# Kernel tuning notes

Hardware: AMD Instinct MI355X
Metric: run time of the kernel (lower is better)

The kernel has to match this reference:

```python
import jax, jax.numpy as jnp
import numpy as np
from jax import lax

SIGMA = 4.0
KS = 2 * int(4.0 * SIGMA + 0.5) + 1  # 33
PAD = KS // 2  # 16


def _gaussian_kernel2d():
    half = (KS - 1) * 0.5
    x = jnp.linspace(-half, half, KS)
    pdf = jnp.exp(-0.5 * (x / SIGMA) ** 2)
    k1 = pdf / pdf.sum()
    # outer product -> dense 2D kernel, shape [O=1, I=1, KS, KS]
    return (k1[:, None] * k1[None, :])[None, None].astype(jnp.float32)


def setup_inputs() -> dict:
    key = jax.random.key(0)
    patch_scores = jax.random.normal(key, (32, 1, 28, 28), dtype=jnp.float32)
    return {
        "patch_scores": patch_scores,
        "blur_w": _gaussian_kernel2d(),
        "img_h": 512,
        "img_w": 512,
    }


def reference(patch_scores, blur_w, img_h, img_w):
    B, C, h, w = patch_scores.shape
    # F.interpolate default mode='nearest': src = floor(dst * in / out)
    ih = (jnp.arange(img_h) * h) // img_h
    iw = (jnp.arange(img_w) * w) // img_w
    x = patch_scores[:, :, ih][:, :, :, iw]  # [B, 1, img_h, img_w]
    # dense 33x33 Gaussian blur conv, padding 16 (same as nn.Conv2d)
    anomaly_map = lax.conv_general_dilated(
        x, blur_w,
        window_strides=(1, 1),
        padding=[(PAD, PAD), (PAD, PAD)],
        dimension_numbers=("NCHW", "OIHW", "NCHW"),
    )
    # mean over channel dim (dim is removed, matching torch.mean(axis=1))
    return anomaly_map.mean(axis=1)  # [B, img_h, img_w]
```

## Files before the change

### kernel.cpp

```cpp
#include <hip/hip_runtime.h>

#define IMG 512
#define PS  28
#define KS  33
#define PAD 16
#define RT  16
#define TILES (IMG / RT)

__device__ __forceinline__ int base_of(int y) {
    int p0 = y - PAD; if (p0 < 0) p0 = 0;
    int b = (p0 * PS) >> 9;
    return b > PS - 3 ? PS - 3 : b;
}

__device__ __forceinline__ float3 collapse(int y, int base, const float* S) {
    float w[3];
#pragma unroll
    for (int d = 0; d < 3; ++d) {
        int s  = base + d;
        int lo = (512 * s + 27) / 28 - y + PAD;
        int hi = (512 * (s + 1) + 27) / 28 - y + PAD;
        lo = min(max(lo, 0), KS);
        hi = min(max(hi, 0), KS);
        w[d] = S[hi] - S[lo];
    }
    return make_float3(w[0], w[1], w[2]);
}

__global__ __launch_bounds__(256) void anomaly_fused(
        const float* __restrict__ p_in,
        const float* __restrict__ blur_w,
        float* __restrict__ out) {
    __shared__ float  S[KS + 1];
    __shared__ __align__(16) float P[PS * PS];
    __shared__ float4 WY[RT];
    __shared__ __align__(16) float N[4][IMG];

    int t    = threadIdx.x;
    int b    = blockIdx.x >> 5;
    int tile = blockIdx.x & (TILES - 1);
    int y0   = tile * RT;
    int smin = base_of(y0);

    if (t < 64) {
        float v = (t < KS) ? blur_w[t * KS + 16] : 0.f;
        float c = __shfl(v, 16);
        float k = v / sqrtf(c);
        float s = k;
#pragma unroll
        for (int d = 1; d <= 32; d <<= 1) {
            float o = __shfl_up(s, (unsigned)d);
            if (t >= d) s += o;
        }
        if (t < KS)  S[t + 1] = s;
        if (t == 33) S[0] = 0.f;
    }
    if (t < (PS * PS) / 4)
        ((float4*)P)[t] = ((const float4*)(p_in + (size_t)b * PS * PS))[t];
    __syncthreads();

    if (t < RT) {
        int by = base_of(y0 + t);
        float3 w = collapse(y0 + t, by, S);
        int  dy = by - smin;
        float u0 = dy ? 0.f : w.x;
        float u1 = dy ? w.x : w.y;
        float u2 = dy ? w.y : w.z;
        float u3 = dy ? w.z : 0.f;
        WY[t] = make_float4(u0, u1, u2, u3);
    }
#pragma unroll
    for (int xi = 0; xi < 2; ++xi) {
        int x = t + xi * 256;
        int bx = base_of(x);
        float3 w = collapse(x, bx, S);
#pragma unroll
        for (int i = 0; i < 4; ++i) {
            int sr = smin + i; if (sr > PS - 1) sr = PS - 1;
            const float* pr = P + sr * PS + bx;
            N[i][x] = w.x * pr[0] + w.y * pr[1] + w.z * pr[2];
        }
    }
    __syncthreads();

    int q    = t & 127;
    int half = t >> 7;
    int x0   = q * 4;

    float4 a0 = *(const float4*)&N[0][x0];
    float4 a1 = *(const float4*)&N[1][x0];
    float4 a2 = *(const float4*)&N[2][x0];
    float4 a3 = *(const float4*)&N[3][x0];

    float* obase = out + ((size_t)b * IMG + y0 + half * 8) * IMG + x0;
#pragma unroll
    for (int r = 0; r < 8; ++r) {
        float4 u = WY[half * 8 + r];
        float4 acc;
        acc.x = u.x * a0.x + u.y * a1.x + u.z * a2.x + u.w * a3.x;
        acc.y = u.x * a0.y + u.y * a1.y + u.z * a2.y + u.w * a3.y;
        acc.z = u.x * a0.z + u.y * a1.z + u.z * a2.z + u.w * a3.z;
        acc.w = u.x * a0.w + u.y * a1.w + u.z * a2.w + u.w * a3.w;
        *(float4*)(obase + (size_t)r * IMG) = acc;
    }
}

extern "C" void kernel_launch(void* const* d_in, const int* in_sizes, int n_in,
                              void* d_out, int out_size, void* d_ws, size_t ws_size,
                              hipStream_t stream) {
    const float* patch = (const float*)d_in[0];
    const float* blur  = (const float*)d_in[1];
    float*       out   = (float*)d_out;

    int B = in_sizes[0] / (PS * PS);
    anomaly_fused<<<B * TILES, 256, 0, stream>>>(patch, blur, out);
}
```

Before: 13.64 us.

## Drop intermediate shared buffer and a barrier; compute row weights via shuffles

Removes the N[4][512] shared-memory intermediate and one __syncthreads. Row weights are now built with wave shuffles straight from the prefix-sum registers, and each thread computes its own four horizontal-collapsed values directly from the patch tile. The output stores become nontemporal. Each thread does somewhat more redundant weight and index arithmetic, with both block halves recomputing the same columns, in exchange for fewer barriers and less LDS traffic.

```diff
diff --git a/kernel.cpp b/kernel.cpp
--- a/kernel.cpp
+++ b/kernel.cpp
@@ -7,24 +7,18 @@
 #define RT  16
 #define TILES (IMG / RT)
 
+typedef float vf4 __attribute__((ext_vector_type(4)));
+
 __device__ __forceinline__ int base_of(int y) {
     int p0 = y - PAD; if (p0 < 0) p0 = 0;
     int b = (p0 * PS) >> 9;
     return b > PS - 3 ? PS - 3 : b;
 }
-
-__device__ __forceinline__ float3 collapse(int y, int base, const float* S) {
-    float w[3];
-#pragma unroll
-    for (int d = 0; d < 3; ++d) {
-        int s  = base + d;
-        int lo = (512 * s + 27) / 28 - y + PAD;
-        int hi = (512 * (s + 1) + 27) / 28 - y + PAD;
-        lo = min(max(lo, 0), KS);
-        hi = min(max(hi, 0), KS);
-        w[d] = S[hi] - S[lo];
-    }
-    return make_float3(w[0], w[1], w[2]);
+__device__ __forceinline__ int C_of(int s) {
+    return (512 * s + 27) / 28;
+}
+__device__ __forceinline__ int clamp33(int i) {
+    return min(max(i, 0), KS);
 }
 
 __global__ __launch_bounds__(256) void anomaly_fused(
@@ -34,7 +28,6 @@
     __shared__ float  S[KS + 1];
     __shared__ __align__(16) float P[PS * PS];
     __shared__ float4 WY[RT];
-    __shared__ __align__(16) float N[4][IMG];
 
     int t    = threadIdx.x;
     int b    = blockIdx.x >> 5;
@@ -42,43 +35,38 @@
     int y0   = tile * RT;
     int smin = base_of(y0);
 
+    if (t < (PS * PS) / 4)
+        ((float4*)P)[t] = ((const float4*)(p_in + (size_t)b * PS * PS))[t];
+
     if (t < 64) {
         float v = (t < KS) ? blur_w[t * KS + 16] : 0.f;
         float c = __shfl(v, 16);
-        float k = v / sqrtf(c);
-        float s = k;
+        float s = v / sqrtf(c);
 #pragma unroll
         for (int d = 1; d <= 32; d <<= 1) {
             float o = __shfl_up(s, (unsigned)d);
             if (t >= d) s += o;
         }
         if (t < KS)  S[t + 1] = s;
-        if (t == 33) S[0] = 0.f;
-    }
-    if (t < (PS * PS) / 4)
-        ((float4*)P)[t] = ((const float4*)(p_in + (size_t)b * PS * PS))[t];
-    __syncthreads();
+        if (t == 63) S[0] = 0.f;
 
-    if (t < RT) {
-        int by = base_of(y0 + t);
-        float3 w = collapse(y0 + t, by, S);
-        int  dy = by - smin;
-        float u0 = dy ? 0.f : w.x;
-        float u1 = dy ? w.x : w.y;
-        float u2 = dy ? w.y : w.z;
-        float u3 = dy ? w.z : 0.f;
-        WY[t] = make_float4(u0, u1, u2, u3);
-    }
-#pragma unroll
-    for (int xi = 0; xi < 2; ++xi) {
-        int x = t + xi * 256;
-        int bx = base_of(x);
-        float3 w = collapse(x, bx, S);
-#pragma unroll
-        for (int i = 0; i < 4; ++i) {
-            int sr = smin + i; if (sr > PS - 1) sr = PS - 1;
-            const float* pr = P + sr * PS + bx;
-            N[i][x] = w.x * pr[0] + w.y * pr[1] + w.z * pr[2];
+        int y  = y0 + (t & (RT - 1));
+        int by = base_of(y);
+        int i0 = clamp33(C_of(by)     - y + PAD);
+        int i1 = clamp33(C_of(by + 1) - y + PAD);
+        int i2 = clamp33(C_of(by + 2) - y + PAD);
+        int i3 = clamp33(C_of(by + 3) - y + PAD);
+        float s0 = (i0 == 0) ? 0.f : __shfl(s, i0 - 1);
+        float s1 = (i1 == 0) ? 0.f : __shfl(s, i1 - 1);
+        float s2 = (i2 == 0) ? 0.f : __shfl(s, i2 - 1);
+        float s3 = (i3 == 0) ? 0.f : __shfl(s, i3 - 1);
+        if (t < RT) {
+            float w0 = s1 - s0, w1 = s2 - s1, w2 = s3 - s2;
+            int dy = by - smin;
+            WY[t] = make_float4(dy ? 0.f : w0,
+                                dy ? w0  : w1,
+                                dy ? w1  : w2,
+                                dy ? w2  : 0.f);
         }
     }
     __syncthreads();
@@ -87,21 +75,44 @@
     int half = t >> 7;
     int x0   = q * 4;
 
-    float4 a0 = *(const float4*)&N[0][x0];
-    float4 a1 = *(const float4*)&N[1][x0];
-    float4 a2 = *(const float4*)&N[2][x0];
-    float4 a3 = *(const float4*)&N[3][x0];
+    float4 u[8];
+#pragma unroll
+    for (int r = 0; r < 8; ++r) u[r] = WY[half * 8 + r];
+
+    float wx[4][3];
+    int   bx[4];
+#pragma unroll
+    for (int j = 0; j < 4; ++j) {
+        int x = x0 + j;
+        bx[j] = base_of(x);
+        int i0 = clamp33(C_of(bx[j])     - x + PAD);
+        int i1 = clamp33(C_of(bx[j] + 1) - x + PAD);
+        int i2 = clamp33(C_of(bx[j] + 2) - x + PAD);
+        int i3 = clamp33(C_of(bx[j] + 3) - x + PAD);
+        float s0 = S[i0], s1 = S[i1], s2 = S[i2], s3 = S[i3];
+        wx[j][0] = s1 - s0; wx[j][1] = s2 - s1; wx[j][2] = s3 - s2;
+    }
+
+    float4 a[4];
+#pragma unroll
+    for (int i = 0; i < 4; ++i) {
+        int sr = smin + i; if (sr > PS - 1) sr = PS - 1;
+        const float* pr = P + sr * PS;
+        a[i].x = wx[0][0]*pr[bx[0]] + wx[0][1]*pr[bx[0]+1] + wx[0][2]*pr[bx[0]+2];
+        a[i].y = wx[1][0]*pr[bx[1]] + wx[1][1]*pr[bx[1]+1] + wx[1][2]*pr[bx[1]+2];
+        a[i].z = wx[2][0]*pr[bx[2]] + wx[2][1]*pr[bx[2]+1] + wx[2][2]*pr[bx[2]+2];
+        a[i].w = wx[3][0]*pr[bx[3]] + wx[3][1]*pr[bx[3]+1] + wx[3][2]*pr[bx[3]+2];
+    }
 
     float* obase = out + ((size_t)b * IMG + y0 + half * 8) * IMG + x0;
 #pragma unroll
     for (int r = 0; r < 8; ++r) {
-        float4 u = WY[half * 8 + r];
-        float4 acc;
-        acc.x = u.x * a0.x + u.y * a1.x + u.z * a2.x + u.w * a3.x;
-        acc.y = u.x * a0.y + u.y * a1.y + u.z * a2.y + u.w * a3.y;
-        acc.z = u.x * a0.z + u.y * a1.z + u.z * a2.z + u.w * a3.z;
-        acc.w = u.x * a0.w + u.y * a1.w + u.z * a2.w + u.w * a3.w;
-        *(float4*)(obase + (size_t)r * IMG) = acc;
+        vf4 acc;
+        acc.x = u[r].x*a[0].x + u[r].y*a[1].x + u[r].z*a[2].x + u[r].w*a[3].x;
+        acc.y = u[r].x*a[0].y + u[r].y*a[1].y + u[r].z*a[2].y + u[r].w*a[3].y;
+        acc.z = u[r].x*a[0].z + u[r].y*a[1].z + u[r].z*a[2].z + u[r].w*a[3].z;
+        acc.w = u[r].x*a[0].w + u[r].y*a[1].w + u[r].z*a[2].w + u[r].w*a[3].w;
+        __builtin_nontemporal_store(acc, (vf4*)(obase + (size_t)r * IMG));
     }
 }
 
```

After: 13.39 us. About the same (-1.8%).
